# Kernel optimization log

Hardware: AMD Instinct MI355X
Metric: run time of the kernel (lower is better)

## Reference

```python
import jax, jax.numpy as jnp
import numpy as np

C = 256
EPS = 1e-5


def setup_inputs() -> dict:
    key = jax.random.key(0)
    ks = jax.random.split(key, 10)
    B, H, W = 4, 64, 64
    x1 = jax.random.normal(ks[0], (B, C, H, W), dtype=jnp.float32)
    x2 = jax.random.normal(ks[1], (B, C, H, W), dtype=jnp.float32)
    s = 1.0 / np.sqrt(C)
    qw = jax.random.normal(ks[2], (C, C), dtype=jnp.float32) * s
    qb = jax.random.normal(ks[3], (C,), dtype=jnp.float32) * 0.01
    kw = jax.random.normal(ks[4], (C, C), dtype=jnp.float32) * s
    kb = jax.random.normal(ks[5], (C,), dtype=jnp.float32) * 0.01
    vw = jax.random.normal(ks[6], (C, C), dtype=jnp.float32) * s
    vb = jax.random.normal(ks[7], (C,), dtype=jnp.float32) * 0.01
    ln_w = jnp.ones((C,), dtype=jnp.float32)
    ln_b = jnp.zeros((C,), dtype=jnp.float32)
    return {"x1": x1, "x2": x2, "qw": qw, "qb": qb, "kw": kw, "kb": kb,
            "vw": vw, "vb": vb, "ln_w": ln_w, "ln_b": ln_b}


def _conv1x1(x, w, b):
    # 1x1 conv == per-pixel matmul over channels. x: [B,C,H,W], w: [O,C]
    return jnp.einsum('oc,bchw->bohw', w, x) + b[None, :, None, None]


def reference(x1, x2, qw, qb, kw, kb, vw, vb, ln_w, ln_b):
    q = _conv1x1(x1, qw, qb)   # [B,C,H,W]
    k = _conv1x1(x2, kw, kb)   # [B,C,H,W]
    v = _conv1x1(x2, vw, vb)   # [B,C,H,W]
    # scores: [B,H,W,I,J]; softmax over LAST axis (j) only, as in the torch code
    scores = jnp.einsum('bchw,bcij->bhwij', q, k)
    attn = jax.nn.softmax(scores, axis=-1)
    fusion = jnp.einsum('bhwij,bcij->bchw', attn, v)  # [B,C,H,W]
    # LayerNorm2d: normalize over channel dim per spatial location
    mean = jnp.mean(fusion, axis=1, keepdims=True)
    var = jnp.var(fusion, axis=1, keepdims=True)
    normed = (fusion - mean) * jax.lax.rsqrt(var + EPS)
    return normed * ln_w[None, :, None, None] + ln_b[None, :, None, None]
```

## Files before the change

kernel.cpp:

```cpp
#include <hip/hip_runtime.h>


#define CDIM 256
#define NPOS 4096
#define BATCH 4
#define EPSV 1e-5f

typedef _Float16 f16;
typedef __attribute__((ext_vector_type(8))) _Float16 f16x8;
typedef __attribute__((ext_vector_type(4))) float f32x4;
typedef __attribute__((ext_vector_type(16))) float f32x16;

#define WST       264
#define QK_STRIDE 264
#define S_STRIDE  68
#define P_STRIDE  72
#define DQ_STRIDE 72


static __device__ __forceinline__ f16x8 cvt8(const float* __restrict__ p) {
    float4 w0 = *(const float4*)p;
    float4 w1 = *(const float4*)(p + 4);
    f16x8 r;
    r[0] = (f16)w0.x; r[1] = (f16)w0.y; r[2] = (f16)w0.z; r[3] = (f16)w0.w;
    r[4] = (f16)w1.x; r[5] = (f16)w1.y; r[6] = (f16)w1.z; r[7] = (f16)w1.w;
    return r;
}

__global__ __launch_bounds__(256, 4) void prep_kernel(
    const float* __restrict__ x1, const float* __restrict__ x2,
    const float* __restrict__ qw, const float* __restrict__ kw,
    const float* __restrict__ vw,
    f16* __restrict__ X1T, f16* __restrict__ X2T, f16* __restrict__ W16)
{
    const int id = blockIdx.x;
    const int t  = threadIdx.x;
    if (id < 2048) {
        __shared__ f16 T[64 * 72];
        const float* xs = (id & 1) ? x2 : x1;
        f16* dst        = (id & 1) ? X2T : X1T;
        const int t2 = id >> 1;
        const int b  = t2 >> 8;
        const int rm = t2 & 255;
        const int c0 = (rm >> 6) * 64;
        const int n0 = (rm & 63) * 64;
        const float* src = xs + ((size_t)b * CDIM + c0) * NPOS + n0;
        const int rr = t >> 6, col = t & 63;
        #pragma unroll
        for (int j = 0; j < 16; ++j) {
            int row = rr + j * 4;
            T[col * 72 + row] = (f16)src[(size_t)row * NPOS + col];
        }
        __syncthreads();
        const int n = t >> 3, lc = (t & 7) * 8;
        f16* d0 = dst + ((size_t)b * NPOS + n0) * CDIM + c0;
        #pragma unroll
        for (int j = 0; j < 2; ++j) {
            int nn = n + j * 32;
            *(f16x8*)(d0 + (size_t)nn * CDIM + lc) = *(const f16x8*)&T[nn * 72 + lc];
        }
    } else {
        const int wblk = id - 2048;
        const int pr = wblk >> 2, h = wblk & 3;
        const float* W = (pr == 0 ? qw : pr == 1 ? kw : vw) + (size_t)h * 64 * CDIM;
        f16* D = W16 + (size_t)pr * CDIM * CDIM + (size_t)h * 64 * CDIM;
        #pragma unroll
        for (int i = 0; i < 8; ++i) {
            int g = t + i * 256;
            int row = g >> 5, col = (g & 31) * 8;
            *(f16x8*)(D + (size_t)row * CDIM + col) = cvt8(W + (size_t)row * CDIM + col);
        }
    }
}

__global__ __launch_bounds__(256, 2) void gemm_kernel(
    const f16* __restrict__ X1T, const f16* __restrict__ X2T,
    const f16* __restrict__ W16,
    const float* __restrict__ qb, const float* __restrict__ kb,
    const float* __restrict__ vb,
    f16* __restrict__ Qg, f16* __restrict__ Kg, f16* __restrict__ Vg)
{
    __shared__ f16 Xs[64 * WST];
    __shared__ f16 Wh[64 * WST];
    __shared__ f16 Ds[64 * DQ_STRIDE];
    __shared__ float biasS[256];

    const int id = blockIdx.x;
    const int pr  = id >> 8;
    const int rem = id & 255;
    const int b   = rem >> 6;
    const int p0  = (rem & 63) << 6;
    const f16* XT = (pr == 0) ? X1T : X2T;
    const f16* Wp = W16 + (size_t)pr * CDIM * CDIM;
    const float* bias = pr == 0 ? qb : pr == 1 ? kb : vb;

    const int t = threadIdx.x, w = t >> 6, l = t & 63, lm = l & 31, lh = l >> 5;
    const int pt = w & 1, ot = w >> 1;

    biasS[t] = bias[t];
    #pragma unroll
    for (int it = 0; it < 8; ++it) {
        int p = w * 16 + it * 2 + lh;
        *(f16x8*)&Xs[p * WST + lm * 8] =
            *(const f16x8*)(XT + ((size_t)(b * NPOS + p0 + p)) * CDIM + lm * 8);
    }

    for (int q = 0; q < 4; ++q) {
        #pragma unroll
        for (int i = 0; i < 8; ++i) {
            int g = t + i * 256;
            int row = g >> 5, col = (g & 31) * 8;
            *(f16x8*)&Wh[row * WST + col] =
                *(const f16x8*)(Wp + (size_t)(q * 64 + row) * CDIM + col);
        }
        __syncthreads();

        f32x16 accA = {}, accB = {};
        #pragma unroll
        for (int ks = 0; ks < 16; ks += 2) {
            f16x8 x0 = *(const f16x8*)&Xs[(pt * 32 + lm) * WST + ks * 16 + lh * 8];
            f16x8 w0 = *(const f16x8*)&Wh[(ot * 32 + lm) * WST + ks * 16 + lh * 8];
            f16x8 x1v = *(const f16x8*)&Xs[(pt * 32 + lm) * WST + (ks + 1) * 16 + lh * 8];
            f16x8 w1 = *(const f16x8*)&Wh[(ot * 32 + lm) * WST + (ks + 1) * 16 + lh * 8];
            if (pr < 2) {
                accA = __builtin_amdgcn_mfma_f32_32x32x16_f16(x0, w0, accA, 0, 0, 0);
                accB = __builtin_amdgcn_mfma_f32_32x32x16_f16(x1v, w1, accB, 0, 0, 0);
            } else {
                accA = __builtin_amdgcn_mfma_f32_32x32x16_f16(w0, x0, accA, 0, 0, 0);
                accB = __builtin_amdgcn_mfma_f32_32x32x16_f16(w1, x1v, accB, 0, 0, 0);
            }
        }

        if (pr < 2) {
            int o_l = ot * 32 + lm;
            float bv = biasS[q * 64 + o_l];
            #pragma unroll
            for (int r = 0; r < 16; ++r) {
                int p_l = pt * 32 + (r & 3) + 8 * (r >> 2) + 4 * lh;
                Ds[p_l * DQ_STRIDE + o_l] = (f16)(accA[r] + accB[r] + bv);
            }
        } else {
            #pragma unroll
            for (int r = 0; r < 16; ++r) {
                int o_l = ot * 32 + (r & 3) + 8 * (r >> 2) + 4 * lh;
                Ds[o_l * DQ_STRIDE + pt * 32 + lm] =
                    (f16)(accA[r] + accB[r] + biasS[q * 64 + o_l]);
            }
        }
        __syncthreads();

        #pragma unroll
        for (int j = 0; j < 2; ++j) {
            int row = (t >> 3) + j * 32;
            int cc  = (t & 7) * 8;
            f16x8 vdat = *(const f16x8*)&Ds[row * DQ_STRIDE + cc];
            if (pr < 2) {
                f16* Out = (pr == 0) ? Qg : Kg;
                *(f16x8*)(Out + ((size_t)(b * NPOS + p0 + row)) * CDIM + q * 64 + cc) = vdat;
            } else {
                *(f16x8*)(Vg + ((size_t)(b * CDIM + q * 64 + row)) * NPOS + p0 + cc) = vdat;
            }
        }
    }
}

__global__ __launch_bounds__(256, 2) void attn_kernel(
    const f16* __restrict__ Qg, const f16* __restrict__ Kg, const f16* __restrict__ Vg,
    const float* __restrict__ ln_w, const float* __restrict__ ln_b,
    float* __restrict__ out)
{
    __shared__ f16   Ks[64 * QK_STRIDE];
    __shared__ float Ss[64 * S_STRIDE];
    __shared__ f16   Ps[64 * P_STRIDE];
    __shared__ float lnw_s[256], lnb_s[256];
    __shared__ float redS[4 * 64], redQ[4 * 64], mu_s[64], rs_s[64];

    const int t  = threadIdx.x;
    const int b  = blockIdx.x >> 6;
    const int p0 = (blockIdx.x & 63) << 6;
    const int w  = t >> 6;
    const int l  = t & 63;
    const int lm = l & 31;
    const int lh = l >> 5;

    lnw_s[t] = ln_w[t];
    lnb_s[t] = ln_b[t];

    const int spt = w & 1;
    const int skt = w >> 1;

    f16x8 qf[16];
    {
        const f16* qptr = Qg + (size_t)(b * NPOS + p0 + spt * 32 + lm) * CDIM + lh * 8;
        #pragma unroll
        for (int ks = 0; ks < 16; ++ks) qf[ks] = *(const f16x8*)(qptr + ks * 16);
    }

    const int kr = t >> 5, koff = (t & 31) * 8;
    f16x8 kreg[8];
    auto issue_k = [&](int ch) {
        const int i0 = ch * 64;
        #pragma unroll
        for (int r = 0; r < 8; ++r)
            kreg[r] = *(const f16x8*)(Kg + (size_t)(b * NPOS + i0 + r * 8 + kr) * CDIM + koff);
    };
    issue_k(0);

    const f16* vbase0 = Vg + (size_t)(b * CDIM + w * 64 + lm) * NPOS;
    const f16* vbase1 = Vg + (size_t)(b * CDIM + w * 64 + 32 + lm) * NPOS;

    f32x16 facc[4] = {};

    for (int ch = 0; ch < 64; ++ch) {
        const int i0 = ch * 64;
        #pragma unroll
        for (int r = 0; r < 8; ++r)
            *(f16x8*)&Ks[(r * 8 + kr) * QK_STRIDE + koff] = kreg[r];
        __syncthreads();

        f16x8 vf0[4], vf1[4];
        #pragma unroll
        for (int ks = 0; ks < 4; ++ks) {
            vf0[ks] = *(const f16x8*)(vbase0 + i0 + ks * 16 + lh * 8);
            vf1[ks] = *(const f16x8*)(vbase1 + i0 + ks * 16 + lh * 8);
        }

        f32x16 sacc = {};
        #pragma unroll
        for (int ks = 0; ks < 16; ++ks) {
            f16x8 bb = *(const f16x8*)&Ks[(skt * 32 + lm) * QK_STRIDE + ks * 16 + lh * 8];
            sacc = __builtin_amdgcn_mfma_f32_32x32x16_f16(qf[ks], bb, sacc, 0, 0, 0);
        }
        #pragma unroll
        for (int r = 0; r < 16; ++r) {
            int row = (r & 3) + 8 * (r >> 2) + 4 * lh;
            Ss[(spt * 32 + row) * S_STRIDE + skt * 32 + lm] = sacc[r];
        }
        __syncthreads();

        {
            const int r  = t >> 2;
            const int sg = (t & 3) * 16;
            const float* srow = &Ss[r * S_STRIDE + sg];
            float v[16];
            f32x4 a0 = *(const f32x4*)(srow);
            f32x4 a1 = *(const f32x4*)(srow + 4);
            f32x4 a2 = *(const f32x4*)(srow + 8);
            f32x4 a3 = *(const f32x4*)(srow + 12);
            v[0]=a0[0]; v[1]=a0[1]; v[2]=a0[2]; v[3]=a0[3];
            v[4]=a1[0]; v[5]=a1[1]; v[6]=a1[2]; v[7]=a1[3];
            v[8]=a2[0]; v[9]=a2[1]; v[10]=a2[2]; v[11]=a2[3];
            v[12]=a3[0]; v[13]=a3[1]; v[14]=a3[2]; v[15]=a3[3];
            float m = v[0];
            #pragma unroll
            for (int i = 1; i < 16; ++i) m = fmaxf(m, v[i]);
            m = fmaxf(m, __shfl_xor(m, 1));
            m = fmaxf(m, __shfl_xor(m, 2));
            float s = 0.f;
            #pragma unroll
            for (int i = 0; i < 16; ++i) { float e = __expf(v[i] - m); v[i] = e; s += e; }
            s += __shfl_xor(s, 1);
            s += __shfl_xor(s, 2);
            float inv = __builtin_amdgcn_rcpf(s);
            f16x8 h0, h1;
            #pragma unroll
            for (int i = 0; i < 8; ++i) { h0[i] = (f16)(v[i] * inv); h1[i] = (f16)(v[i + 8] * inv); }
            *(f16x8*)&Ps[r * P_STRIDE + sg]     = h0;
            *(f16x8*)&Ps[r * P_STRIDE + sg + 8] = h1;
        }
        __syncthreads();

        if (ch < 63) issue_k(ch + 1);

        #pragma unroll
        for (int ks = 0; ks < 4; ++ks) {
            f16x8 bp0 = *(const f16x8*)&Ps[lm * P_STRIDE + ks * 16 + lh * 8];
            f16x8 bp1 = *(const f16x8*)&Ps[(32 + lm) * P_STRIDE + ks * 16 + lh * 8];
            facc[0] = __builtin_amdgcn_mfma_f32_32x32x16_f16(vf0[ks], bp0, facc[0], 0, 0, 0);
            facc[1] = __builtin_amdgcn_mfma_f32_32x32x16_f16(vf0[ks], bp1, facc[1], 0, 0, 0);
            facc[2] = __builtin_amdgcn_mfma_f32_32x32x16_f16(vf1[ks], bp0, facc[2], 0, 0, 0);
            facc[3] = __builtin_amdgcn_mfma_f32_32x32x16_f16(vf1[ks], bp1, facc[3], 0, 0, 0);
        }
    }

    float ps0 = 0.f, ps1 = 0.f, pq0 = 0.f, pq1 = 0.f;
    #pragma unroll
    for (int ii = 0; ii < 2; ++ii) {
        #pragma unroll
        for (int r = 0; r < 16; ++r) {
            float a = facc[ii * 2 + 0][r];
            float c = facc[ii * 2 + 1][r];
            ps0 += a; pq0 += a * a;
            ps1 += c; pq1 += c * c;
        }
    }
    ps0 += __shfl_xor(ps0, 32); pq0 += __shfl_xor(pq0, 32);
    ps1 += __shfl_xor(ps1, 32); pq1 += __shfl_xor(pq1, 32);
    if (lh == 0) {
        redS[w * 64 + lm] = ps0;        redQ[w * 64 + lm] = pq0;
        redS[w * 64 + 32 + lm] = ps1;   redQ[w * 64 + 32 + lm] = pq1;
    }
    __syncthreads();
    if (t < 64) {
        float s = redS[t] + redS[64 + t] + redS[128 + t] + redS[192 + t];
        float q = redQ[t] + redQ[64 + t] + redQ[128 + t] + redQ[192 + t];
        float mean = s * (1.0f / 256.0f);
        float var  = q * (1.0f / 256.0f) - mean * mean;
        mu_s[t] = mean;
        rs_s[t] = rsqrtf(var + EPSV);
    }
    __syncthreads();
    #pragma unroll
    for (int ii = 0; ii < 2; ++ii) {
        #pragma unroll
        for (int jj = 0; jj < 2; ++jj) {
            int p = jj * 32 + lm;
            float mu = mu_s[p], rs = rs_s[p];
            float* dst = out + (size_t)b * CDIM * NPOS + p0 + p;
            #pragma unroll
            for (int r = 0; r < 16; ++r) {
                int c = w * 64 + ii * 32 + (r & 3) + 8 * (r >> 2) + 4 * lh;
                float vL = facc[ii * 2 + jj][r];
                dst[(size_t)c * NPOS] = (vL - mu) * rs * lnw_s[c] + lnb_s[c];
            }
        }
    }
}

extern "C" void kernel_launch(void* const* d_in, const int* in_sizes, int n_in,
                              void* d_out, int out_size, void* d_ws, size_t ws_size,
                              hipStream_t stream)
{
    const float* x1  = (const float*)d_in[0];
    const float* x2  = (const float*)d_in[1];
    const float* qw  = (const float*)d_in[2];
    const float* qb  = (const float*)d_in[3];
    const float* kw  = (const float*)d_in[4];
    const float* kb  = (const float*)d_in[5];
    const float* vw  = (const float*)d_in[6];
    const float* vb  = (const float*)d_in[7];
    const float* lnw = (const float*)d_in[8];
    const float* lnb = (const float*)d_in[9];

    const size_t tsz = (size_t)BATCH * NPOS * CDIM;
    f16* Qg  = (f16*)d_ws;
    f16* Kg  = Qg + tsz;
    f16* Vg  = Kg + tsz;
    f16* X1T = Vg + tsz;
    f16* X2T = X1T + tsz;
    f16* W16 = X2T + tsz;

    prep_kernel<<<2060, 256, 0, stream>>>(x1, x2, qw, kw, vw, X1T, X2T, W16);
    gemm_kernel<<<768, 256, 0, stream>>>(X1T, X2T, W16, qb, kb, vb, Qg, Kg, Vg);
    attn_kernel<<<256, 256, 0, stream>>>(Qg, Kg, Vg, lnw, lnb, (float*)d_out);
}
```

Before: 248.2 us.

## Split attention key loop across two 256-thread groups per block

The attention kernel now runs 512 threads per block as two groups that each own alternate 64-key chunks, with separate shared-memory buffers for K, scores and probabilities. Each group accumulates a partial output, and the second group's partials are added into the first group's through shared memory before LayerNorm. This doubles the waves working on each of the 256 blocks, which only fill the GPU's compute units once, so more latency can be hidden. The cost is double the shared memory, an extra reduction pass and a __syncthreads that now spans both groups.

```diff
diff --git a/kernel.cpp b/kernel.cpp
--- a/kernel.cpp
+++ b/kernel.cpp
@@ -16,6 +16,7 @@
 #define S_STRIDE  68
 #define P_STRIDE  72
 #define DQ_STRIDE 72
+#define FT_STRIDE 66
 
 
 static __device__ __forceinline__ f16x8 cvt8(const float* __restrict__ p) {
@@ -164,30 +165,32 @@
     }
 }
 
-__global__ __launch_bounds__(256, 2) void attn_kernel(
+__global__ __launch_bounds__(512, 1) void attn_kernel(
     const f16* __restrict__ Qg, const f16* __restrict__ Kg, const f16* __restrict__ Vg,
     const float* __restrict__ ln_w, const float* __restrict__ ln_b,
     float* __restrict__ out)
 {
-    __shared__ f16   Ks[64 * QK_STRIDE];
-    __shared__ float Ss[64 * S_STRIDE];
-    __shared__ f16   Ps[64 * P_STRIDE];
+    __shared__ f16   Ks[2][64 * QK_STRIDE];
+    __shared__ float Ss[2][64 * S_STRIDE];
+    __shared__ f16   Ps[2][64 * P_STRIDE];
     __shared__ float lnw_s[256], lnb_s[256];
     __shared__ float redS[4 * 64], redQ[4 * 64], mu_s[64], rs_s[64];
 
-    const int t  = threadIdx.x;
-    const int b  = blockIdx.x >> 6;
-    const int p0 = (blockIdx.x & 63) << 6;
-    const int w  = t >> 6;
-    const int l  = t & 63;
-    const int lm = l & 31;
-    const int lh = l >> 5;
-
-    lnw_s[t] = ln_w[t];
-    lnb_s[t] = ln_b[t];
-
-    const int spt = w & 1;
-    const int skt = w >> 1;
+    const int t   = threadIdx.x;
+    const int b   = blockIdx.x >> 6;
+    const int p0  = (blockIdx.x & 63) << 6;
+    const int w   = t >> 6;
+    const int g   = t >> 8;
+    const int wl  = w & 3;
+    const int tl  = t & 255;
+    const int l   = t & 63;
+    const int lm  = l & 31;
+    const int lh  = l >> 5;
+
+    if (t < 256) { lnw_s[t] = ln_w[t]; lnb_s[t] = ln_b[t]; }
+
+    const int spt = wl & 1;
+    const int skt = wl >> 1;
 
     f16x8 qf[16];
     {
@@ -196,7 +199,7 @@
         for (int ks = 0; ks < 16; ++ks) qf[ks] = *(const f16x8*)(qptr + ks * 16);
     }
 
-    const int kr = t >> 5, koff = (t & 31) * 8;
+    const int kr = tl >> 5, koff = (tl & 31) * 8;
     f16x8 kreg[8];
     auto issue_k = [&](int ch) {
         const int i0 = ch * 64;
@@ -204,18 +207,20 @@
         for (int r = 0; r < 8; ++r)
             kreg[r] = *(const f16x8*)(Kg + (size_t)(b * NPOS + i0 + r * 8 + kr) * CDIM + koff);
     };
-    issue_k(0);
-
-    const f16* vbase0 = Vg + (size_t)(b * CDIM + w * 64 + lm) * NPOS;
-    const f16* vbase1 = Vg + (size_t)(b * CDIM + w * 64 + 32 + lm) * NPOS;
+    issue_k(g);
+
+    const f16* vbase0 = Vg + (size_t)(b * CDIM + wl * 64 + lm) * NPOS;
+    const f16* vbase1 = Vg + (size_t)(b * CDIM + wl * 64 + 32 + lm) * NPOS;
 
     f32x16 facc[4] = {};
 
-    for (int ch = 0; ch < 64; ++ch) {
+    for (int it = 0; it < 32; ++it) {
+        const int ch = it * 2 + g;
         const int i0 = ch * 64;
+
         #pragma unroll
         for (int r = 0; r < 8; ++r)
-            *(f16x8*)&Ks[(r * 8 + kr) * QK_STRIDE + koff] = kreg[r];
+            *(f16x8*)&Ks[g][(r * 8 + kr) * QK_STRIDE + koff] = kreg[r];
         __syncthreads();
 
         f16x8 vf0[4], vf1[4];
@@ -228,20 +233,20 @@
         f32x16 sacc = {};
         #pragma unroll
         for (int ks = 0; ks < 16; ++ks) {
-            f16x8 bb = *(const f16x8*)&Ks[(skt * 32 + lm) * QK_STRIDE + ks * 16 + lh * 8];
+            f16x8 bb = *(const f16x8*)&Ks[g][(skt * 32 + lm) * QK_STRIDE + ks * 16 + lh * 8];
             sacc = __builtin_amdgcn_mfma_f32_32x32x16_f16(qf[ks], bb, sacc, 0, 0, 0);
         }
         #pragma unroll
         for (int r = 0; r < 16; ++r) {
             int row = (r & 3) + 8 * (r >> 2) + 4 * lh;
-            Ss[(spt * 32 + row) * S_STRIDE + skt * 32 + lm] = sacc[r];
+            Ss[g][(spt * 32 + row) * S_STRIDE + skt * 32 + lm] = sacc[r];
         }
         __syncthreads();
 
         {
-            const int r  = t >> 2;
-            const int sg = (t & 3) * 16;
-            const float* srow = &Ss[r * S_STRIDE + sg];
+            const int r  = tl >> 2;
+            const int sg = (tl & 3) * 16;
+            const float* srow = &Ss[g][r * S_STRIDE + sg];
             float v[16];
             f32x4 a0 = *(const f32x4*)(srow);
             f32x4 a1 = *(const f32x4*)(srow + 4);
@@ -265,17 +270,17 @@
             f16x8 h0, h1;
             #pragma unroll
             for (int i = 0; i < 8; ++i) { h0[i] = (f16)(v[i] * inv); h1[i] = (f16)(v[i + 8] * inv); }
-            *(f16x8*)&Ps[r * P_STRIDE + sg]     = h0;
-            *(f16x8*)&Ps[r * P_STRIDE + sg + 8] = h1;
-        }
-        __syncthreads();
-
-        if (ch < 63) issue_k(ch + 1);
+            *(f16x8*)&Ps[g][r * P_STRIDE + sg]     = h0;
+            *(f16x8*)&Ps[g][r * P_STRIDE + sg + 8] = h1;
+        }
+        __syncthreads();
+
+        if (it < 31) issue_k(ch + 2);
 
         #pragma unroll
         for (int ks = 0; ks < 4; ++ks) {
-            f16x8 bp0 = *(const f16x8*)&Ps[lm * P_STRIDE + ks * 16 + lh * 8];
-            f16x8 bp1 = *(const f16x8*)&Ps[(32 + lm) * P_STRIDE + ks * 16 + lh * 8];
+            f16x8 bp0 = *(const f16x8*)&Ps[g][lm * P_STRIDE + ks * 16 + lh * 8];
+            f16x8 bp1 = *(const f16x8*)&Ps[g][(32 + lm) * P_STRIDE + ks * 16 + lh * 8];
             facc[0] = __builtin_amdgcn_mfma_f32_32x32x16_f16(vf0[ks], bp0, facc[0], 0, 0, 0);
             facc[1] = __builtin_amdgcn_mfma_f32_32x32x16_f16(vf0[ks], bp1, facc[1], 0, 0, 0);
             facc[2] = __builtin_amdgcn_mfma_f32_32x32x16_f16(vf1[ks], bp0, facc[2], 0, 0, 0);
@@ -283,22 +288,49 @@
         }
     }
 
+    float* Ftmp = (float*)&Ks[0][0];
+    __syncthreads();
+    if (g == 1) {
+        #pragma unroll
+        for (int ii = 0; ii < 2; ++ii)
+            #pragma unroll
+            for (int jj = 0; jj < 2; ++jj)
+                #pragma unroll
+                for (int r = 0; r < 16; ++r) {
+                    int c = wl * 64 + ii * 32 + (r & 3) + 8 * (r >> 2) + 4 * lh;
+                    int p = jj * 32 + lm;
+                    Ftmp[c * FT_STRIDE + p] = facc[ii * 2 + jj][r];
+                }
+    }
+    __syncthreads();
     float ps0 = 0.f, ps1 = 0.f, pq0 = 0.f, pq1 = 0.f;
-    #pragma unroll
-    for (int ii = 0; ii < 2; ++ii) {
-        #pragma unroll
-        for (int r = 0; r < 16; ++r) {
-            float a = facc[ii * 2 + 0][r];
-            float c = facc[ii * 2 + 1][r];
-            ps0 += a; pq0 += a * a;
-            ps1 += c; pq1 += c * c;
-        }
-    }
-    ps0 += __shfl_xor(ps0, 32); pq0 += __shfl_xor(pq0, 32);
-    ps1 += __shfl_xor(ps1, 32); pq1 += __shfl_xor(pq1, 32);
-    if (lh == 0) {
-        redS[w * 64 + lm] = ps0;        redQ[w * 64 + lm] = pq0;
-        redS[w * 64 + 32 + lm] = ps1;   redQ[w * 64 + 32 + lm] = pq1;
+    if (g == 0) {
+        #pragma unroll
+        for (int ii = 0; ii < 2; ++ii)
+            #pragma unroll
+            for (int jj = 0; jj < 2; ++jj)
+                #pragma unroll
+                for (int r = 0; r < 16; ++r) {
+                    int c = wl * 64 + ii * 32 + (r & 3) + 8 * (r >> 2) + 4 * lh;
+                    int p = jj * 32 + lm;
+                    facc[ii * 2 + jj][r] += Ftmp[c * FT_STRIDE + p];
+                }
+        #pragma unroll
+        for (int ii = 0; ii < 2; ++ii) {
+            #pragma unroll
+            for (int r = 0; r < 16; ++r) {
+                float a = facc[ii * 2 + 0][r];
+                float c = facc[ii * 2 + 1][r];
+                ps0 += a; pq0 += a * a;
+                ps1 += c; pq1 += c * c;
+            }
+        }
+        ps0 += __shfl_xor(ps0, 32); pq0 += __shfl_xor(pq0, 32);
+        ps1 += __shfl_xor(ps1, 32); pq1 += __shfl_xor(pq1, 32);
+        if (lh == 0) {
+            redS[wl * 64 + lm] = ps0;        redQ[wl * 64 + lm] = pq0;
+            redS[wl * 64 + 32 + lm] = ps1;   redQ[wl * 64 + 32 + lm] = pq1;
+        }
     }
     __syncthreads();
     if (t < 64) {
@@ -310,18 +342,20 @@
         rs_s[t] = rsqrtf(var + EPSV);
     }
     __syncthreads();
-    #pragma unroll
-    for (int ii = 0; ii < 2; ++ii) {
-        #pragma unroll
-        for (int jj = 0; jj < 2; ++jj) {
-            int p = jj * 32 + lm;
-            float mu = mu_s[p], rs = rs_s[p];
-            float* dst = out + (size_t)b * CDIM * NPOS + p0 + p;
-            #pragma unroll
-            for (int r = 0; r < 16; ++r) {
-                int c = w * 64 + ii * 32 + (r & 3) + 8 * (r >> 2) + 4 * lh;
-                float vL = facc[ii * 2 + jj][r];
-                dst[(size_t)c * NPOS] = (vL - mu) * rs * lnw_s[c] + lnb_s[c];
+    if (g == 0) {
+        #pragma unroll
+        for (int ii = 0; ii < 2; ++ii) {
+            #pragma unroll
+            for (int jj = 0; jj < 2; ++jj) {
+                int p = jj * 32 + lm;
+                float mu = mu_s[p], rs = rs_s[p];
+                float* dst = out + (size_t)b * CDIM * NPOS + p0 + p;
+                #pragma unroll
+                for (int r = 0; r < 16; ++r) {
+                    int c = wl * 64 + ii * 32 + (r & 3) + 8 * (r >> 2) + 4 * lh;
+                    float vL = facc[ii * 2 + jj][r];
+                    dst[(size_t)c * NPOS] = (vL - mu) * rs * lnw_s[c] + lnb_s[c];
+                }
             }
         }
     }
@@ -352,5 +386,5 @@
 
     prep_kernel<<<2060, 256, 0, stream>>>(x1, x2, qw, kw, vw, X1T, X2T, W16);
     gemm_kernel<<<768, 256, 0, stream>>>(X1T, X2T, W16, qb, kb, vb, Qg, Kg, Vg);
-    attn_kernel<<<256, 256, 0, stream>>>(Qg, Kg, Vg, lnw, lnb, (float*)d_out);
-}
+    attn_kernel<<<256, 512, 0, stream>>>(Qg, Kg, Vg, lnw, lnb, (float*)d_out);
+}
```

Result: faster. 229.9 us (-7.4%).
